# Optimization experiments

Hardware: AMD Instinct MI355X
Metric: run time of the kernel (lower is better)

## Reference

```python
import jax, jax.numpy as jnp
import numpy as np

B = 16384   # batch (agents x parallel envs)
IN = 12     # input_dim
H = 64      # hidden_dim -> 2H = 128
OUT = 25    # output_dim (forced by x[:,0:5]..x[:,20:25] slicing)


def setup_inputs() -> dict:
    key = jax.random.key(0)
    ks = jax.random.split(key, 24)
    n = lambda k, s: jax.random.normal(k, s, dtype=jnp.float32)
    s = 0.1  # scale params to keep SiLU/softmax in a sane range
    return {
        "x": n(ks[0], (B, IN)),
        "na": 4,
        # mlp_in: Linear(IN, 2H) + SiLU
        "W_in": n(ks[1], (2 * H, IN)) * s, "b_in": n(ks[2], (2 * H,)) * s,
        # first attention (2H)
        "Aq4": n(ks[3], (2 * H, 2 * H)) * s, "Bq4": n(ks[4], (2 * H,)) * s,
        "Ak4": n(ks[5], (2 * H, 2 * H)) * s, "Bk4": n(ks[6], (2 * H,)) * s,
        "Av4": n(ks[7], (2 * H, 2 * H)) * s, "Bv4": n(ks[8], (2 * H,)) * s,
        # mlp_hidden_4: Linear(2H, H) + SiLU
        "W_h": n(ks[9], (H, 2 * H)) * s, "b_h": n(ks[10], (H,)) * s,
        # second attention (H)
        "Aq7": n(ks[11], (H, H)) * s, "Bq7": n(ks[12], (H,)) * s,
        "Ak7": n(ks[13], (H, H)) * s, "Bk7": n(ks[14], (H,)) * s,
        "Av7": n(ks[15], (H, H)) * s, "Bv7": n(ks[16], (H,)) * s,
        # mlp_out: Linear(H, OUT) + SiLU
        "W_out": n(ks[17], (OUT, H)) * s, "b_out": n(ks[18], (OUT,)) * s,
    }


def _attn(h, Aq, Bq, Ak, Bk, Av, Bv):
    # h: [B, D]; torch does bmm(A, x^T)+B with x of shape [B,1,D] -> seq-len-1
    # attention, i.e. scores are an outer product q k^T of shape [B, D, D].
    q = jax.nn.silu(h @ Aq.T + Bq)                      # [B, D]
    k = jax.nn.silu(h @ Ak.T + Bk)                      # [B, D]
    v = jax.nn.silu(h @ Av.T + Bv)                      # [B, D]
    a = jax.nn.softmax(q[:, :, None] * k[:, None, :], axis=2)  # [B, D, D]
    return jax.nn.silu(jnp.einsum("bij,bj->bi", a, v))  # [B, D]


def reference(x, na, W_in, b_in, Aq4, Bq4, Ak4, Bk4, Av4, Bv4,
              W_h, b_h, Aq7, Bq7, Ak7, Bk7, Av7, Bv7, W_out, b_out):
    h = jax.nn.silu(x @ W_in.T + b_in)                  # [B, 2H]
    h = _attn(h, Aq4, Bq4, Ak4, Bk4, Av4, Bv4)          # [B, 2H]
    h = jax.nn.silu(h @ W_h.T + b_h)                    # [B, H]
    h = _attn(h, Aq7, Bq7, Ak7, Bk7, Av7, Bv7)          # [B, H]
    y = jax.nn.silu(h @ W_out.T + b_out)                # [B, 25]

    # block-diagonal quadratic-form assembly (l=2, kron with ones(1,2))
    M11 = jnp.sum(y[:, 0:5] ** 2, axis=1)               # [B]
    M12 = jnp.sum(y[:, 5:10] ** 2, axis=1)
    M21 = jnp.sum(y[:, 10:15] ** 2, axis=1)
    M22 = jnp.sum(y[:, 15:20] ** 2, axis=1)
    Mpp = jnp.sum(y[:, 20:25] ** 2, axis=1)             # [B]
    q = y[:, :4]                                        # [B, 4] = [q0,q1,q2,q3]
    # M = [[diag(M11), diag(M12)],[diag(M21), diag(M22)]] (each 2x2 diag)
    quad = (M11 * (q[:, 0] ** 2 + q[:, 1] ** 2)
            + (M12 + M21) * (q[:, 0] * q[:, 2] + q[:, 1] * q[:, 3])
            + M22 * (q[:, 2] ** 2 + q[:, 3] ** 2))
    return (quad + Mpp)[:, None]                        # [B, 1]
```

## Files before the change

kernel.cpp:

```cpp
#include <hip/hip_runtime.h>

#define RPW 4
#define WAVES 4
#define RPB (RPW * WAVES)
#define NM 14

using short8 = __attribute__((ext_vector_type(8))) short;
using f32x4  = __attribute__((ext_vector_type(4))) float;

#define LOG2E 1.4426950408889634f

static __device__ __forceinline__ float ex2(float x) { return __builtin_amdgcn_exp2f(x); }
static __device__ __forceinline__ float rcpf_(float x) { return __builtin_amdgcn_rcpf(x); }
static __device__ __forceinline__ float silu_(float x) {
    return x * rcpf_(1.0f + ex2(-x * LOG2E));
}
static __device__ __forceinline__ unsigned short bfhi(float x) {
    return (unsigned short)(__float_as_uint(x) >> 16);
}
static __device__ __forceinline__ unsigned short bfrn(float x) {
    unsigned u = __float_as_uint(x);
    return (unsigned short)((u + 0x7fffu + ((u >> 16) & 1u)) >> 16);
}
static __device__ __forceinline__ float bf2f(unsigned short h) {
    return __uint_as_float(((unsigned)h) << 16);
}

template <int CTRL>
static __device__ __forceinline__ float dpp_rot(float v) {
    return __uint_as_float(
        __builtin_amdgcn_update_dpp(0u, __float_as_uint(v), CTRL, 0xF, 0xF, true));
}
static __device__ __forceinline__ float rsum16(float v) {
    v += dpp_rot<0x128>(v);
    v += dpp_rot<0x124>(v);
    v += dpp_rot<0x122>(v);
    v += dpp_rot<0x121>(v);
    return v;
}

__constant__ float c_invfact[15] = {
    1.f, 1.f, 0.5f, 1.f/6, 1.f/24, 1.f/120, 1.f/720, 1.f/5040, 1.f/40320,
    1.f/362880, 1.f/3628800, 1.f/39916800, 1.f/479001600,
    1.f/6227020800.f, 1.f/87178291200.f};

template <int O, int I>
__device__ __forceinline__ void tr(const float* __restrict__ s, float* __restrict__ d,
                                   int t0, int stride) {
    for (int idx = t0; idx < O * I; idx += stride) {
        int o = idx / I, in = idx - o * I;
        d[in * O + o] = s[idx];
    }
}
template <int N>
__device__ __forceinline__ void cvt(const float* __restrict__ s,
                                    unsigned short* __restrict__ hi,
                                    unsigned short* __restrict__ lo,
                                    int t0, int stride) {
    for (int i = t0; i < N; i += stride) {
        float a = s[i];
        unsigned short h = bfhi(a);
        float r = a - bf2f(h);
        hi[i] = h;
        lo[i] = bfhi(r);
    }
}

__global__ void tweights(const float* __restrict__ s0, const float* __restrict__ s1,
                         const float* __restrict__ s2, const float* __restrict__ s3,
                         const float* __restrict__ s4, const float* __restrict__ s5,
                         const float* __restrict__ s6, const float* __restrict__ s7,
                         const float* __restrict__ s8, float* __restrict__ ws) {
    const int stride = gridDim.x * blockDim.x;
    const int t0 = blockIdx.x * blockDim.x + threadIdx.x;
    tr<128, 12>(s0, ws + 0, t0, stride);
    unsigned short* u4 = (unsigned short*)(ws + 1536);
    cvt<128 * 128>(s1, u4 + 0,     u4 + 16384, t0, stride);
    cvt<128 * 128>(s2, u4 + 32768, u4 + 49152, t0, stride);
    cvt<128 * 128>(s3, u4 + 65536, u4 + 81920, t0, stride);
    unsigned short* wh = (unsigned short*)(ws + 50688);
    cvt<64 * 128>(s4, wh + 0, wh + 8192, t0, stride);
    unsigned short* u7 = (unsigned short*)(ws + 58880);
    cvt<64 * 64>(s5, u7 + 0,     u7 + 4096,  t0, stride);
    cvt<64 * 64>(s6, u7 + 8192,  u7 + 12288, t0, stride);
    cvt<64 * 64>(s7, u7 + 16384, u7 + 20480, t0, stride);
    tr<25, 64>(s8, ws + 71168, t0, stride);
}

__global__ __launch_bounds__(256, 4) void fused_net(
    const float* __restrict__ x, const float* __restrict__ ws,
    const float* __restrict__ b_in,
    const float* __restrict__ Bq4, const float* __restrict__ Bk4, const float* __restrict__ Bv4,
    const float* __restrict__ b_h,
    const float* __restrict__ Bq7, const float* __restrict__ Bk7, const float* __restrict__ Bv7,
    const float* __restrict__ b_out,
    float* __restrict__ out) {
    __shared__ __align__(16) unsigned short hAhi[16][136], hAlo[16][136];
    __shared__ __align__(16) unsigned short h2hi[16][80],  h2lo[16][80];
    __shared__ __align__(16) float sQ[16][132];
    __shared__ __align__(16) unsigned short sKVb[16][132][2];
    __shared__ __align__(16) float h3T[WAVES][64][RPW];
    __shared__ __align__(16) float sXT[WAVES][12][RPW];
    __shared__ __align__(16) float sY[WAVES][RPW][26];

    const int tid = threadIdx.x;
    const int w = tid >> 6;
    const int l = tid & 63;
    const int row0 = blockIdx.x * RPB + w * RPW;
    const int m16 = l & 15, quad = l >> 4;
    const int g = l & 15, r = l >> 4;
    const int R = w * RPW + r;

    const float* WinT  = ws + 0;
    const float* WoutT = ws + 71168;

    if (l < 12 * RPW) {
        float v = x[row0 * 12 + l];
        int rr = l / 12, in = l - rr * 12;
        sXT[w][in][rr] = v;
    }

    {
        float2 bb = *(const float2*)&b_in[2 * l];
        float a0[RPW], a1[RPW];
        #pragma unroll
        for (int rr = 0; rr < RPW; rr++) { a0[rr] = bb.x; a1[rr] = bb.y; }
        #pragma unroll
        for (int in = 0; in < 12; in++) {
            float2 wv = *(const float2*)&WinT[in * 128 + 2 * l];
            float4 xr = *(const float4*)&sXT[w][in][0];
            a0[0] = fmaf(xr.x, wv.x, a0[0]); a1[0] = fmaf(xr.x, wv.y, a1[0]);
            a0[1] = fmaf(xr.y, wv.x, a0[1]); a1[1] = fmaf(xr.y, wv.y, a1[1]);
            a0[2] = fmaf(xr.z, wv.x, a0[2]); a1[2] = fmaf(xr.z, wv.y, a1[2]);
            a0[3] = fmaf(xr.w, wv.x, a0[3]); a1[3] = fmaf(xr.w, wv.y, a1[3]);
        }
        #pragma unroll
        for (int rr = 0; rr < RPW; rr++) {
            float h0 = silu_(a0[rr]), h1 = silu_(a1[rr]);
            unsigned short h0h = bfhi(h0), h1h = bfhi(h1);
            float r0 = h0 - bf2f(h0h), r1 = h1 - bf2f(h1h);
            *(unsigned*)&hAhi[w * 4 + rr][2 * l] = (unsigned)h0h | ((unsigned)h1h << 16);
            *(unsigned*)&hAlo[w * 4 + rr][2 * l] = (unsigned)bfhi(r0) | ((unsigned)bfhi(r1) << 16);
        }
    }
    __syncthreads();

    {
        short8 Ah[4], Al[4];
        #pragma unroll
        for (int kt = 0; kt < 4; kt++) {
            Ah[kt] = *(const short8*)&hAhi[m16][kt * 32 + quad * 8];
            Al[kt] = *(const short8*)&hAlo[m16][kt * 32 + quad * 8];
        }
        const unsigned short* u4 = (const unsigned short*)(ws + 1536);
        #pragma unroll
        for (int t = 0; t < 6; t++) {
            const int nt = w * 6 + t;
            const int mat = nt >> 3;
            const int n = (nt & 7) * 16 + m16;
            const float* bp = (mat == 0) ? Bq4 : (mat == 1) ? Bk4 : Bv4;
            float b = bp[n];
            f32x4 acc = {b, b, b, b};
            const unsigned short* Bh = u4 + mat * 32768 + n * 128;
            const unsigned short* Bl = Bh + 16384;
            #pragma unroll
            for (int kt = 0; kt < 4; kt++) {
                short8 bh = *(const short8*)&Bh[kt * 32 + quad * 8];
                short8 bl = *(const short8*)&Bl[kt * 32 + quad * 8];
                acc = __builtin_amdgcn_mfma_f32_16x16x32_bf16(Ah[kt], bh, acc, 0, 0, 0);
                acc = __builtin_amdgcn_mfma_f32_16x16x32_bf16(Ah[kt], bl, acc, 0, 0, 0);
                acc = __builtin_amdgcn_mfma_f32_16x16x32_bf16(Al[kt], bh, acc, 0, 0, 0);
            }
            #pragma unroll
            for (int reg = 0; reg < 4; reg++) {
                int row = quad * 4 + reg;
                float val = silu_(acc[reg]);
                if (mat == 0)      sQ[row][n] = val;
                else if (mat == 1) sKVb[row][n][0] = bfrn(val);
                else               sKVb[row][n][1] = bfrn(val);
            }
        }
    }
    __syncthreads();

    {
        float dmom[NM];
        float nmom[NM + 1];
        #pragma unroll
        for (int m = 0; m < NM; m++) dmom[m] = 0.f;
        #pragma unroll
        for (int m = 0; m <= NM; m++) nmom[m] = 0.f;
        uint4 u0 = *(const uint4*)&sKVb[R][g * 8][0];
        uint4 u1 = *(const uint4*)&sKVb[R][g * 8 + 4][0];
        unsigned us[8] = {u0.x, u0.y, u0.z, u0.w, u1.x, u1.y, u1.z, u1.w};
        #pragma unroll
        for (int jj = 0; jj < 8; jj++) {
            unsigned u = us[jj];
            float kf = __uint_as_float(u << 16);
            float vf = __uint_as_float(u & 0xffff0000u);
            nmom[0] += vf;
            float p = kf;
            dmom[0] += p; nmom[1] = fmaf(vf, p, nmom[1]);
            #pragma unroll
            for (int m = 1; m < NM; m++) {
                p *= kf;
                dmom[m] += p;
                nmom[m + 1] = fmaf(vf, p, nmom[m + 1]);
            }
        }
        #pragma unroll
        for (int m = 0; m < NM; m++) dmom[m] = rsum16(dmom[m]);
        #pragma unroll
        for (int m = 0; m <= NM; m++) nmom[m] = rsum16(nmom[m]);
        float cd[NM + 1], cn[NM + 1];
        cd[0] = 128.f; cn[0] = nmom[0];
        #pragma unroll
        for (int m = 1; m <= NM; m++) {
            cd[m] = dmom[m - 1] * c_invfact[m];
            cn[m] = nmom[m] * c_invfact[m];
        }
        float4 qa = *(const float4*)&sQ[R][g * 8];
        float4 qb = *(const float4*)&sQ[R][g * 8 + 4];
        float qs[8] = {qa.x, qa.y, qa.z, qa.w, qb.x, qb.y, qb.z, qb.w};
        unsigned hiw[4], low[4];
        #pragma unroll
        for (int i = 0; i < 8; i++) {
            float t = qs[i];
            float d = cd[NM], nn = cn[NM];
            #pragma unroll
            for (int m = NM - 1; m >= 0; m--) {
                d = fmaf(d, t, cd[m]);
                nn = fmaf(nn, t, cn[m]);
            }
            float o = silu_(nn * rcpf_(d));
            unsigned short oh = bfhi(o);
            unsigned short olo = bfhi(o - bf2f(oh));
            if (i & 1) { hiw[i >> 1] |= ((unsigned)oh) << 16; low[i >> 1] |= ((unsigned)olo) << 16; }
            else       { hiw[i >> 1] = oh; low[i >> 1] = olo; }
        }
        *(uint4*)&hAhi[R][g * 8] = make_uint4(hiw[0], hiw[1], hiw[2], hiw[3]);
        *(uint4*)&hAlo[R][g * 8] = make_uint4(low[0], low[1], low[2], low[3]);
    }
    __syncthreads();

    {
        short8 Ah[4], Al[4];
        #pragma unroll
        for (int kt = 0; kt < 4; kt++) {
            Ah[kt] = *(const short8*)&hAhi[m16][kt * 32 + quad * 8];
            Al[kt] = *(const short8*)&hAlo[m16][kt * 32 + quad * 8];
        }
        const unsigned short* whh = (const unsigned short*)(ws + 50688);
        const unsigned short* whl = whh + 8192;
        const int n = w * 16 + m16;
        float b = b_h[n];
        f32x4 acc = {b, b, b, b};
        #pragma unroll
        for (int kt = 0; kt < 4; kt++) {
            short8 bh = *(const short8*)&whh[n * 128 + kt * 32 + quad * 8];
            short8 bl = *(const short8*)&whl[n * 128 + kt * 32 + quad * 8];
            acc = __builtin_amdgcn_mfma_f32_16x16x32_bf16(Ah[kt], bh, acc, 0, 0, 0);
            acc = __builtin_amdgcn_mfma_f32_16x16x32_bf16(Ah[kt], bl, acc, 0, 0, 0);
            acc = __builtin_amdgcn_mfma_f32_16x16x32_bf16(Al[kt], bh, acc, 0, 0, 0);
        }
        #pragma unroll
        for (int reg = 0; reg < 4; reg++) {
            int row = quad * 4 + reg;
            float hv = silu_(acc[reg]);
            unsigned short hh = bfhi(hv);
            h2hi[row][n] = hh;
            h2lo[row][n] = bfhi(hv - bf2f(hh));
        }
    }
    __syncthreads();

    {
        short8 Ah[2], Al[2];
        #pragma unroll
        for (int kt = 0; kt < 2; kt++) {
            Ah[kt] = *(const short8*)&h2hi[m16][kt * 32 + quad * 8];
            Al[kt] = *(const short8*)&h2lo[m16][kt * 32 + quad * 8];
        }
        const unsigned short* u7 = (const unsigned short*)(ws + 58880);
        #pragma unroll
        for (int t = 0; t < 3; t++) {
            const int nt = w * 3 + t;
            const int mat = nt >> 2;
            const int n = (nt & 3) * 16 + m16;
            const float* bp = (mat == 0) ? Bq7 : (mat == 1) ? Bk7 : Bv7;
            float b = bp[n];
            f32x4 acc = {b, b, b, b};
            const unsigned short* Bh = u7 + mat * 8192 + n * 64;
            const unsigned short* Bl = Bh + 4096;
            #pragma unroll
            for (int kt = 0; kt < 2; kt++) {
                short8 bh = *(const short8*)&Bh[kt * 32 + quad * 8];
                short8 bl = *(const short8*)&Bl[kt * 32 + quad * 8];
                acc = __builtin_amdgcn_mfma_f32_16x16x32_bf16(Ah[kt], bh, acc, 0, 0, 0);
                acc = __builtin_amdgcn_mfma_f32_16x16x32_bf16(Ah[kt], bl, acc, 0, 0, 0);
                acc = __builtin_amdgcn_mfma_f32_16x16x32_bf16(Al[kt], bh, acc, 0, 0, 0);
            }
            #pragma unroll
            for (int reg = 0; reg < 4; reg++) {
                int row = quad * 4 + reg;
                float val = silu_(acc[reg]);
                if (mat == 0)      sQ[row][n] = val;
                else if (mat == 1) sKVb[row][n][0] = bfrn(val);
                else               sKVb[row][n][1] = bfrn(val);
            }
        }
    }
    __syncthreads();

    {
        float dmom[NM];
        float nmom[NM + 1];
        #pragma unroll
        for (int m = 0; m < NM; m++) dmom[m] = 0.f;
        #pragma unroll
        for (int m = 0; m <= NM; m++) nmom[m] = 0.f;
        uint4 u0 = *(const uint4*)&sKVb[R][g * 4][0];
        unsigned us[4] = {u0.x, u0.y, u0.z, u0.w};
        #pragma unroll
        for (int jj = 0; jj < 4; jj++) {
            unsigned u = us[jj];
            float kf = __uint_as_float(u << 16);
            float vf = __uint_as_float(u & 0xffff0000u);
            nmom[0] += vf;
            float p = kf;
            dmom[0] += p; nmom[1] = fmaf(vf, p, nmom[1]);
            #pragma unroll
            for (int m = 1; m < NM; m++) {
                p *= kf;
                dmom[m] += p;
                nmom[m + 1] = fmaf(vf, p, nmom[m + 1]);
            }
        }
        #pragma unroll
        for (int m = 0; m < NM; m++) dmom[m] = rsum16(dmom[m]);
        #pragma unroll
        for (int m = 0; m <= NM; m++) nmom[m] = rsum16(nmom[m]);
        float cd[NM + 1], cn[NM + 1];
        cd[0] = 64.f; cn[0] = nmom[0];
        #pragma unroll
        for (int m = 1; m <= NM; m++) {
            cd[m] = dmom[m - 1] * c_invfact[m];
            cn[m] = nmom[m] * c_invfact[m];
        }
        float4 qa = *(const float4*)&sQ[R][g * 4];
        float qs[4] = {qa.x, qa.y, qa.z, qa.w};
        #pragma unroll
        for (int i = 0; i < 4; i++) {
            float t = qs[i];
            float d = cd[NM], nn = cn[NM];
            #pragma unroll
            for (int m = NM - 1; m >= 0; m--) {
                d = fmaf(d, t, cd[m]);
                nn = fmaf(nn, t, cn[m]);
            }
            h3T[w][g * 4 + i][r] = silu_(nn * rcpf_(d));
        }
    }

    {
        const int o = l & 31;
        const int half = l >> 5;
        const int oc = (o < 25) ? o : 0;
        float y[RPW];
        float bb = (half == 0) ? b_out[oc] : 0.f;
        #pragma unroll
        for (int rr = 0; rr < RPW; rr++) y[rr] = bb;
        const int in0 = half * 32;
        #pragma unroll 4
        for (int i = 0; i < 32; i++) {
            int in = in0 + i;
            float wv = WoutT[in * 25 + oc];
            float4 xr = *(const float4*)&h3T[w][in][0];
            y[0] = fmaf(xr.x, wv, y[0]);
            y[1] = fmaf(xr.y, wv, y[1]);
            y[2] = fmaf(xr.z, wv, y[2]);
            y[3] = fmaf(xr.w, wv, y[3]);
        }
        #pragma unroll
        for (int rr = 0; rr < RPW; rr++) {
            float full = y[rr] + __shfl_xor(y[rr], 32, 64);
            if (l < 25) sY[w][rr][l] = silu_(full);
        }
    }

    if (l < RPW) {
        const int rr = l;
        float y[25];
        #pragma unroll
        for (int c = 0; c < 25; c++) y[c] = sY[w][rr][c];
        float M11 = 0.f, M12 = 0.f, M21 = 0.f, M22 = 0.f, Mpp = 0.f;
        #pragma unroll
        for (int c = 0; c < 5; c++) {
            M11 = fmaf(y[c], y[c], M11);
            M12 = fmaf(y[5 + c], y[5 + c], M12);
            M21 = fmaf(y[10 + c], y[10 + c], M21);
            M22 = fmaf(y[15 + c], y[15 + c], M22);
            Mpp = fmaf(y[20 + c], y[20 + c], Mpp);
        }
        float quad = M11 * (y[0] * y[0] + y[1] * y[1])
                   + (M12 + M21) * (y[0] * y[2] + y[1] * y[3])
                   + M22 * (y[2] * y[2] + y[3] * y[3]);
        out[row0 + rr] = quad + Mpp;
    }
}

extern "C" void kernel_launch(void* const* d_in, const int* in_sizes, int n_in,
                              void* d_out, int out_size, void* d_ws, size_t ws_size,
                              hipStream_t stream) {
    const float* x    = (const float*)d_in[0];
    const float* W_in = (const float*)d_in[2];
    const float* b_in = (const float*)d_in[3];
    const float* Aq4  = (const float*)d_in[4];
    const float* Bq4  = (const float*)d_in[5];
    const float* Ak4  = (const float*)d_in[6];
    const float* Bk4  = (const float*)d_in[7];
    const float* Av4  = (const float*)d_in[8];
    const float* Bv4  = (const float*)d_in[9];
    const float* W_h  = (const float*)d_in[10];
    const float* b_h  = (const float*)d_in[11];
    const float* Aq7  = (const float*)d_in[12];
    const float* Bq7  = (const float*)d_in[13];
    const float* Ak7  = (const float*)d_in[14];
    const float* Bk7  = (const float*)d_in[15];
    const float* Av7  = (const float*)d_in[16];
    const float* Bv7  = (const float*)d_in[17];
    const float* Wout = (const float*)d_in[18];
    const float* bout = (const float*)d_in[19];
    float* ws = (float*)d_ws;

    tweights<<<256, 256, 0, stream>>>(W_in, Aq4, Ak4, Av4, W_h, Aq7, Ak7, Av7, Wout, ws);

    const int B = in_sizes[0] / 12;
    const int grid = B / RPB;
    fused_net<<<grid, 256, 0, stream>>>(x, ws, b_in, Bq4, Bk4, Bv4,
                                        b_h, Bq7, Bk7, Bv7, bout, (float*)d_out);
}
```

Baseline: 134.7 us.

## Shrink blocks to two waves with eight rows and prefetch MFMA weight fragments

Blocks drop from 4 waves/16 rows to 2 waves/8 rows, doubling the grid. MFMA tiles now carry only 8 valid rows (duplicated via m16&7), and only half the lanes write results. The first weight fragments of each GEMM stage are prefetched early, and the W_h GEMM is merged into the preceding attention section behind an extra barrier. Accumulation is split across two accumulators to shorten MFMA dependency chains. This halves useful MFMA work per instruction, so total MFMA issue roughly doubles, traded for more blocks and better latency hiding.

```diff
diff --git a/kernel.cpp b/kernel.cpp
--- a/kernel.cpp
+++ b/kernel.cpp
@@ -1,7 +1,7 @@
 #include <hip/hip_runtime.h>
 
 #define RPW 4
-#define WAVES 4
+#define WAVES 2
 #define RPB (RPW * WAVES)
 #define NM 14
 
@@ -87,7 +87,7 @@
     tr<25, 64>(s8, ws + 71168, t0, stride);
 }
 
-__global__ __launch_bounds__(256, 4) void fused_net(
+__global__ __launch_bounds__(128, 4) void fused_net(
     const float* __restrict__ x, const float* __restrict__ ws,
     const float* __restrict__ b_in,
     const float* __restrict__ Bq4, const float* __restrict__ Bk4, const float* __restrict__ Bv4,
@@ -95,10 +95,10 @@
     const float* __restrict__ Bq7, const float* __restrict__ Bk7, const float* __restrict__ Bv7,
     const float* __restrict__ b_out,
     float* __restrict__ out) {
-    __shared__ __align__(16) unsigned short hAhi[16][136], hAlo[16][136];
-    __shared__ __align__(16) unsigned short h2hi[16][80],  h2lo[16][80];
-    __shared__ __align__(16) float sQ[16][132];
-    __shared__ __align__(16) unsigned short sKVb[16][132][2];
+    __shared__ __align__(16) unsigned short hAhi[8][136], hAlo[8][136];
+    __shared__ __align__(16) unsigned short h2hi[8][80],  h2lo[8][80];
+    __shared__ __align__(16) float sQ[8][132];
+    __shared__ __align__(16) unsigned short sKVb[8][132][2];
     __shared__ __align__(16) float h3T[WAVES][64][RPW];
     __shared__ __align__(16) float sXT[WAVES][12][RPW];
     __shared__ __align__(16) float sY[WAVES][RPW][26];
@@ -113,11 +113,26 @@
 
     const float* WinT  = ws + 0;
     const float* WoutT = ws + 71168;
+    const unsigned short* u4 = (const unsigned short*)(ws + 1536);
 
     if (l < 12 * RPW) {
         float v = x[row0 * 12 + l];
         int rr = l / 12, in = l - rr * 12;
         sXT[w][in][rr] = v;
+    }
+
+    short8 p2bh[4], p2bl[4];
+    {
+        const int nt = w * 12;
+        const int mat = nt >> 3;
+        const int n = (nt & 7) * 16 + m16;
+        const unsigned short* Bh = u4 + mat * 32768 + n * 128;
+        const unsigned short* Bl = Bh + 16384;
+        #pragma unroll
+        for (int kt = 0; kt < 4; kt++) {
+            p2bh[kt] = *(const short8*)&Bh[kt * 32 + quad * 8];
+            p2bl[kt] = *(const short8*)&Bl[kt * 32 + quad * 8];
+        }
     }
 
     {
@@ -149,41 +164,69 @@
         short8 Ah[4], Al[4];
         #pragma unroll
         for (int kt = 0; kt < 4; kt++) {
-            Ah[kt] = *(const short8*)&hAhi[m16][kt * 32 + quad * 8];
-            Al[kt] = *(const short8*)&hAlo[m16][kt * 32 + quad * 8];
-        }
-        const unsigned short* u4 = (const unsigned short*)(ws + 1536);
-        #pragma unroll
-        for (int t = 0; t < 6; t++) {
-            const int nt = w * 6 + t;
+            Ah[kt] = *(const short8*)&hAhi[m16 & 7][kt * 32 + quad * 8];
+            Al[kt] = *(const short8*)&hAlo[m16 & 7][kt * 32 + quad * 8];
+        }
+        #pragma unroll 4
+        for (int t = 0; t < 12; t++) {
+            const int nt = w * 12 + t;
             const int mat = nt >> 3;
             const int n = (nt & 7) * 16 + m16;
             const float* bp = (mat == 0) ? Bq4 : (mat == 1) ? Bk4 : Bv4;
             float b = bp[n];
-            f32x4 acc = {b, b, b, b};
+            f32x4 acc0 = {b, b, b, b};
+            f32x4 acc1 = {0.f, 0.f, 0.f, 0.f};
             const unsigned short* Bh = u4 + mat * 32768 + n * 128;
             const unsigned short* Bl = Bh + 16384;
+            short8 bh[4], bl[4];
+            if (t == 0) {
+                #pragma unroll
+                for (int kt = 0; kt < 4; kt++) { bh[kt] = p2bh[kt]; bl[kt] = p2bl[kt]; }
+            } else {
+                #pragma unroll
+                for (int kt = 0; kt < 4; kt++) {
+                    bh[kt] = *(const short8*)&Bh[kt * 32 + quad * 8];
+                    bl[kt] = *(const short8*)&Bl[kt * 32 + quad * 8];
+                }
+            }
             #pragma unroll
             for (int kt = 0; kt < 4; kt++) {
-                short8 bh = *(const short8*)&Bh[kt * 32 + quad * 8];
-                short8 bl = *(const short8*)&Bl[kt * 32 + quad * 8];
-                acc = __builtin_amdgcn_mfma_f32_16x16x32_bf16(Ah[kt], bh, acc, 0, 0, 0);
-                acc = __builtin_amdgcn_mfma_f32_16x16x32_bf16(Ah[kt], bl, acc, 0, 0, 0);
-                acc = __builtin_amdgcn_mfma_f32_16x16x32_bf16(Al[kt], bh, acc, 0, 0, 0);
-            }
-            #pragma unroll
-            for (int reg = 0; reg < 4; reg++) {
-                int row = quad * 4 + reg;
-                float val = silu_(acc[reg]);
-                if (mat == 0)      sQ[row][n] = val;
-                else if (mat == 1) sKVb[row][n][0] = bfrn(val);
-                else               sKVb[row][n][1] = bfrn(val);
+                if (kt & 1) {
+                    acc1 = __builtin_amdgcn_mfma_f32_16x16x32_bf16(Ah[kt], bh[kt], acc1, 0, 0, 0);
+                    acc1 = __builtin_amdgcn_mfma_f32_16x16x32_bf16(Ah[kt], bl[kt], acc1, 0, 0, 0);
+                    acc1 = __builtin_amdgcn_mfma_f32_16x16x32_bf16(Al[kt], bh[kt], acc1, 0, 0, 0);
+                } else {
+                    acc0 = __builtin_amdgcn_mfma_f32_16x16x32_bf16(Ah[kt], bh[kt], acc0, 0, 0, 0);
+                    acc0 = __builtin_amdgcn_mfma_f32_16x16x32_bf16(Ah[kt], bl[kt], acc0, 0, 0, 0);
+                    acc0 = __builtin_amdgcn_mfma_f32_16x16x32_bf16(Al[kt], bh[kt], acc0, 0, 0, 0);
+                }
+            }
+            if (quad < 2) {
+                #pragma unroll
+                for (int reg = 0; reg < 4; reg++) {
+                    int row = quad * 4 + reg;
+                    float val = silu_(acc0[reg] + acc1[reg]);
+                    if (mat == 0)      sQ[row][n] = val;
+                    else if (mat == 1) sKVb[row][n][0] = bfrn(val);
+                    else               sKVb[row][n][1] = bfrn(val);
+                }
             }
         }
     }
     __syncthreads();
 
     {
+        short8 p4bh[4], p4bl[4];
+        const unsigned short* whh = (const unsigned short*)(ws + 50688);
+        const unsigned short* whl = whh + 8192;
+        {
+            const int n4 = (w * 2) * 16 + m16;
+            #pragma unroll
+            for (int kt = 0; kt < 4; kt++) {
+                p4bh[kt] = *(const short8*)&whh[n4 * 128 + kt * 32 + quad * 8];
+                p4bl[kt] = *(const short8*)&whl[n4 * 128 + kt * 32 + quad * 8];
+            }
+        }
         float dmom[NM];
         float nmom[NM + 1];
         #pragma unroll
@@ -240,73 +283,95 @@
         }
         *(uint4*)&hAhi[R][g * 8] = make_uint4(hiw[0], hiw[1], hiw[2], hiw[3]);
         *(uint4*)&hAlo[R][g * 8] = make_uint4(low[0], low[1], low[2], low[3]);
+        __syncthreads();
+
+        short8 Ah[4], Al[4];
+        #pragma unroll
+        for (int kt = 0; kt < 4; kt++) {
+            Ah[kt] = *(const short8*)&hAhi[m16 & 7][kt * 32 + quad * 8];
+            Al[kt] = *(const short8*)&hAlo[m16 & 7][kt * 32 + quad * 8];
+        }
+        #pragma unroll
+        for (int t = 0; t < 2; t++) {
+            const int n = (w * 2 + t) * 16 + m16;
+            short8 bh[4], bl[4];
+            if (t == 0) {
+                #pragma unroll
+                for (int kt = 0; kt < 4; kt++) { bh[kt] = p4bh[kt]; bl[kt] = p4bl[kt]; }
+            } else {
+                #pragma unroll
+                for (int kt = 0; kt < 4; kt++) {
+                    bh[kt] = *(const short8*)&whh[n * 128 + kt * 32 + quad * 8];
+                    bl[kt] = *(const short8*)&whl[n * 128 + kt * 32 + quad * 8];
+                }
+            }
+            float b = b_h[n];
+            f32x4 acc0 = {b, b, b, b};
+            f32x4 acc1 = {0.f, 0.f, 0.f, 0.f};
+            #pragma unroll
+            for (int kt = 0; kt < 4; kt++) {
+                if (kt & 1) {
+                    acc1 = __builtin_amdgcn_mfma_f32_16x16x32_bf16(Ah[kt], bh[kt], acc1, 0, 0, 0);
+                    acc1 = __builtin_amdgcn_mfma_f32_16x16x32_bf16(Ah[kt], bl[kt], acc1, 0, 0, 0);
+                    acc1 = __builtin_amdgcn_mfma_f32_16x16x32_bf16(Al[kt], bh[kt], acc1, 0, 0, 0);
+                } else {
+                    acc0 = __builtin_amdgcn_mfma_f32_16x16x32_bf16(Ah[kt], bh[kt], acc0, 0, 0, 0);
+                    acc0 = __builtin_amdgcn_mfma_f32_16x16x32_bf16(Ah[kt], bl[kt], acc0, 0, 0, 0);
+                    acc0 = __builtin_amdgcn_mfma_f32_16x16x32_bf16(Al[kt], bh[kt], acc0, 0, 0, 0);
+                }
+            }
+            if (quad < 2) {
+                #pragma unroll
+                for (int reg = 0; reg < 4; reg++) {
+                    int row = quad * 4 + reg;
+                    float hv = silu_(acc0[reg] + acc1[reg]);
+                    unsigned short hh = bfhi(hv);
+                    h2hi[row][n] = hh;
+                    h2lo[row][n] = bfhi(hv - bf2f(hh));
+                }
+            }
+        }
     }
     __syncthreads();
 
     {
-        short8 Ah[4], Al[4];
-        #pragma unroll
-        for (int kt = 0; kt < 4; kt++) {
-            Ah[kt] = *(const short8*)&hAhi[m16][kt * 32 + quad * 8];
-            Al[kt] = *(const short8*)&hAlo[m16][kt * 32 + quad * 8];
-        }
-        const unsigned short* whh = (const unsigned short*)(ws + 50688);
-        const unsigned short* whl = whh + 8192;
-        const int n = w * 16 + m16;
-        float b = b_h[n];
-        f32x4 acc = {b, b, b, b};
-        #pragma unroll
-        for (int kt = 0; kt < 4; kt++) {
-            short8 bh = *(const short8*)&whh[n * 128 + kt * 32 + quad * 8];
-            short8 bl = *(const short8*)&whl[n * 128 + kt * 32 + quad * 8];
-            acc = __builtin_amdgcn_mfma_f32_16x16x32_bf16(Ah[kt], bh, acc, 0, 0, 0);
-            acc = __builtin_amdgcn_mfma_f32_16x16x32_bf16(Ah[kt], bl, acc, 0, 0, 0);
-            acc = __builtin_amdgcn_mfma_f32_16x16x32_bf16(Al[kt], bh, acc, 0, 0, 0);
-        }
-        #pragma unroll
-        for (int reg = 0; reg < 4; reg++) {
-            int row = quad * 4 + reg;
-            float hv = silu_(acc[reg]);
-            unsigned short hh = bfhi(hv);
-            h2hi[row][n] = hh;
-            h2lo[row][n] = bfhi(hv - bf2f(hh));
-        }
-    }
-    __syncthreads();
-
-    {
+        const unsigned short* u7 = (const unsigned short*)(ws + 58880);
         short8 Ah[2], Al[2];
         #pragma unroll
         for (int kt = 0; kt < 2; kt++) {
-            Ah[kt] = *(const short8*)&h2hi[m16][kt * 32 + quad * 8];
-            Al[kt] = *(const short8*)&h2lo[m16][kt * 32 + quad * 8];
-        }
-        const unsigned short* u7 = (const unsigned short*)(ws + 58880);
-        #pragma unroll
-        for (int t = 0; t < 3; t++) {
-            const int nt = w * 3 + t;
+            Ah[kt] = *(const short8*)&h2hi[m16 & 7][kt * 32 + quad * 8];
+            Al[kt] = *(const short8*)&h2lo[m16 & 7][kt * 32 + quad * 8];
+        }
+        #pragma unroll 3
+        for (int t = 0; t < 6; t++) {
+            const int nt = w * 6 + t;
             const int mat = nt >> 2;
             const int n = (nt & 3) * 16 + m16;
             const float* bp = (mat == 0) ? Bq7 : (mat == 1) ? Bk7 : Bv7;
             float b = bp[n];
-            f32x4 acc = {b, b, b, b};
+            f32x4 acc0 = {b, b, b, b};
+            f32x4 acc1 = {0.f, 0.f, 0.f, 0.f};
             const unsigned short* Bh = u7 + mat * 8192 + n * 64;
             const unsigned short* Bl = Bh + 4096;
-            #pragma unroll
-            for (int kt = 0; kt < 2; kt++) {
-                short8 bh = *(const short8*)&Bh[kt * 32 + quad * 8];
-                short8 bl = *(const short8*)&Bl[kt * 32 + quad * 8];
-                acc = __builtin_amdgcn_mfma_f32_16x16x32_bf16(Ah[kt], bh, acc, 0, 0, 0);
-                acc = __builtin_amdgcn_mfma_f32_16x16x32_bf16(Ah[kt], bl, acc, 0, 0, 0);
-                acc = __builtin_amdgcn_mfma_f32_16x16x32_bf16(Al[kt], bh, acc, 0, 0, 0);
-            }
-            #pragma unroll
-            for (int reg = 0; reg < 4; reg++) {
-                int row = quad * 4 + reg;
-                float val = silu_(acc[reg]);
-                if (mat == 0)      sQ[row][n] = val;
-                else if (mat == 1) sKVb[row][n][0] = bfrn(val);
-                else               sKVb[row][n][1] = bfrn(val);
+            short8 bh0 = *(const short8*)&Bh[quad * 8];
+            short8 bl0 = *(const short8*)&Bl[quad * 8];
+            short8 bh1 = *(const short8*)&Bh[32 + quad * 8];
+            short8 bl1 = *(const short8*)&Bl[32 + quad * 8];
+            acc0 = __builtin_amdgcn_mfma_f32_16x16x32_bf16(Ah[0], bh0, acc0, 0, 0, 0);
+            acc1 = __builtin_amdgcn_mfma_f32_16x16x32_bf16(Ah[1], bh1, acc1, 0, 0, 0);
+            acc0 = __builtin_amdgcn_mfma_f32_16x16x32_bf16(Ah[0], bl0, acc0, 0, 0, 0);
+            acc1 = __builtin_amdgcn_mfma_f32_16x16x32_bf16(Ah[1], bl1, acc1, 0, 0, 0);
+            acc0 = __builtin_amdgcn_mfma_f32_16x16x32_bf16(Al[0], bh0, acc0, 0, 0, 0);
+            acc1 = __builtin_amdgcn_mfma_f32_16x16x32_bf16(Al[1], bh1, acc1, 0, 0, 0);
+            if (quad < 2) {
+                #pragma unroll
+                for (int reg = 0; reg < 4; reg++) {
+                    int row = quad * 4 + reg;
+                    float val = silu_(acc0[reg] + acc1[reg]);
+                    if (mat == 0)      sQ[row][n] = val;
+                    else if (mat == 1) sKVb[row][n][0] = bfrn(val);
+                    else               sKVb[row][n][1] = bfrn(val);
+                }
             }
         }
     }
@@ -402,10 +467,10 @@
             M22 = fmaf(y[15 + c], y[15 + c], M22);
             Mpp = fmaf(y[20 + c], y[20 + c], Mpp);
         }
-        float quad = M11 * (y[0] * y[0] + y[1] * y[1])
-                   + (M12 + M21) * (y[0] * y[2] + y[1] * y[3])
-                   + M22 * (y[2] * y[2] + y[3] * y[3]);
-        out[row0 + rr] = quad + Mpp;
+        float quad_ = M11 * (y[0] * y[0] + y[1] * y[1])
+                    + (M12 + M21) * (y[0] * y[2] + y[1] * y[3])
+                    + M22 * (y[2] * y[2] + y[3] * y[3]);
+        out[row0 + rr] = quad_ + Mpp;
     }
 }
 
@@ -437,6 +502,6 @@
 
     const int B = in_sizes[0] / 12;
     const int grid = B / RPB;
-    fused_net<<<grid, 256, 0, stream>>>(x, ws, b_in, Bq4, Bk4, Bv4,
+    fused_net<<<grid, 128, 0, stream>>>(x, ws, b_in, Bq4, Bk4, Bv4,
                                         b_h, Bq7, Bk7, Bv7, bout, (float*)d_out);
 }
```

New measurement: 163.2 us. 21.2% more time.

## Interleave two 16-row groups per block to overlap MFMA and moment phases

Applied to the files above, without the earlier changes.

Each block now processes two 16-row groups with double-buffered shared memory, and a skewed schedule runs the MFMA phase of one group alongside the scalar moment/polynomial phase of the other between barriers. MFMA chains are split into two accumulators to shorten dependency chains. The Taylor moment order is reduced from 14 to 12, and launch bounds are relaxed to 2 blocks per SM, giving more registers but halving the grid. The risks are lower occupancy, doubled LDS use, and reduced accuracy of the truncated series.

```diff
diff --git a/kernel.cpp b/kernel.cpp
--- a/kernel.cpp
+++ b/kernel.cpp
@@ -1,9 +1,6 @@
 #include <hip/hip_runtime.h>
 
-#define RPW 4
-#define WAVES 4
-#define RPB (RPW * WAVES)
-#define NM 14
+#define NM 12
 
 using short8 = __attribute__((ext_vector_type(8))) short;
 using f32x4  = __attribute__((ext_vector_type(4))) float;
@@ -39,10 +36,11 @@
     return v;
 }
 
-__constant__ float c_invfact[15] = {
+__constant__ float c_invfact[13] = {
     1.f, 1.f, 0.5f, 1.f/6, 1.f/24, 1.f/120, 1.f/720, 1.f/5040, 1.f/40320,
-    1.f/362880, 1.f/3628800, 1.f/39916800, 1.f/479001600,
-    1.f/6227020800.f, 1.f/87178291200.f};
+    1.f/362880, 1.f/3628800, 1.f/39916800, 1.f/479001600};
+
+#define MFMA16(A, B, C) __builtin_amdgcn_mfma_f32_16x16x32_bf16((A), (B), (C), 0, 0, 0)
 
 template <int O, int I>
 __device__ __forceinline__ void tr(const float* __restrict__ s, float* __restrict__ d,
@@ -87,7 +85,7 @@
     tr<25, 64>(s8, ws + 71168, t0, stride);
 }
 
-__global__ __launch_bounds__(256, 4) void fused_net(
+__global__ __launch_bounds__(256, 2) void fused_net(
     const float* __restrict__ x, const float* __restrict__ ws,
     const float* __restrict__ b_in,
     const float* __restrict__ Bq4, const float* __restrict__ Bk4, const float* __restrict__ Bv4,
@@ -95,64 +93,67 @@
     const float* __restrict__ Bq7, const float* __restrict__ Bk7, const float* __restrict__ Bv7,
     const float* __restrict__ b_out,
     float* __restrict__ out) {
-    __shared__ __align__(16) unsigned short hAhi[16][136], hAlo[16][136];
-    __shared__ __align__(16) unsigned short h2hi[16][80],  h2lo[16][80];
-    __shared__ __align__(16) float sQ[16][132];
-    __shared__ __align__(16) unsigned short sKVb[16][132][2];
-    __shared__ __align__(16) float h3T[WAVES][64][RPW];
-    __shared__ __align__(16) float sXT[WAVES][12][RPW];
-    __shared__ __align__(16) float sY[WAVES][RPW][26];
+    __shared__ __align__(16) unsigned short hAhi[2][16][136], hAlo[2][16][136];
+    __shared__ __align__(16) unsigned short h2hi[2][16][80],  h2lo[2][16][80];
+    __shared__ __align__(16) float sQ[2][16][132];
+    __shared__ __align__(16) unsigned short sKVb[2][16][132][2];
+    __shared__ __align__(16) float h3T[2][4][64][4];
+    __shared__ __align__(16) float sXT[2][4][12][4];
+    __shared__ __align__(16) float sY[2][4][4][26];
 
     const int tid = threadIdx.x;
     const int w = tid >> 6;
     const int l = tid & 63;
-    const int row0 = blockIdx.x * RPB + w * RPW;
+    const int row0 = blockIdx.x * 32;
     const int m16 = l & 15, quad = l >> 4;
     const int g = l & 15, r = l >> 4;
-    const int R = w * RPW + r;
+    const int R = w * 4 + r;
 
     const float* WinT  = ws + 0;
     const float* WoutT = ws + 71168;
-
-    if (l < 12 * RPW) {
-        float v = x[row0 * 12 + l];
-        int rr = l / 12, in = l - rr * 12;
-        sXT[w][in][rr] = v;
-    }
-
-    {
+    const unsigned short* u4  = (const unsigned short*)(ws + 1536);
+    const unsigned short* whh = (const unsigned short*)(ws + 50688);
+    const unsigned short* whl = whh + 8192;
+    const unsigned short* u7  = (const unsigned short*)(ws + 58880);
+
+    auto stageX = [&](int G) {
+        if (l < 48) {
+            int rr = l / 12, in = l - rr * 12;
+            sXT[G][w][in][rr] = x[(row0 + G * 16 + w * 4 + rr) * 12 + in];
+        }
+    };
+
+    auto phase1 = [&](int G) {
         float2 bb = *(const float2*)&b_in[2 * l];
-        float a0[RPW], a1[RPW];
-        #pragma unroll
-        for (int rr = 0; rr < RPW; rr++) { a0[rr] = bb.x; a1[rr] = bb.y; }
+        float a0[4], a1[4];
+        #pragma unroll
+        for (int rr = 0; rr < 4; rr++) { a0[rr] = bb.x; a1[rr] = bb.y; }
         #pragma unroll
         for (int in = 0; in < 12; in++) {
             float2 wv = *(const float2*)&WinT[in * 128 + 2 * l];
-            float4 xr = *(const float4*)&sXT[w][in][0];
+            float4 xr = *(const float4*)&sXT[G][w][in][0];
             a0[0] = fmaf(xr.x, wv.x, a0[0]); a1[0] = fmaf(xr.x, wv.y, a1[0]);
             a0[1] = fmaf(xr.y, wv.x, a0[1]); a1[1] = fmaf(xr.y, wv.y, a1[1]);
             a0[2] = fmaf(xr.z, wv.x, a0[2]); a1[2] = fmaf(xr.z, wv.y, a1[2]);
             a0[3] = fmaf(xr.w, wv.x, a0[3]); a1[3] = fmaf(xr.w, wv.y, a1[3]);
         }
         #pragma unroll
-        for (int rr = 0; rr < RPW; rr++) {
+        for (int rr = 0; rr < 4; rr++) {
             float h0 = silu_(a0[rr]), h1 = silu_(a1[rr]);
             unsigned short h0h = bfhi(h0), h1h = bfhi(h1);
             float r0 = h0 - bf2f(h0h), r1 = h1 - bf2f(h1h);
-            *(unsigned*)&hAhi[w * 4 + rr][2 * l] = (unsigned)h0h | ((unsigned)h1h << 16);
-            *(unsigned*)&hAlo[w * 4 + rr][2 * l] = (unsigned)bfhi(r0) | ((unsigned)bfhi(r1) << 16);
-        }
-    }
-    __syncthreads();
-
-    {
+            *(unsigned*)&hAhi[G][w * 4 + rr][2 * l] = (unsigned)h0h | ((unsigned)h1h << 16);
+            *(unsigned*)&hAlo[G][w * 4 + rr][2 * l] = (unsigned)bfhi(r0) | ((unsigned)bfhi(r1) << 16);
+        }
+    };
+
+    auto phase2 = [&](int G) {
         short8 Ah[4], Al[4];
         #pragma unroll
         for (int kt = 0; kt < 4; kt++) {
-            Ah[kt] = *(const short8*)&hAhi[m16][kt * 32 + quad * 8];
-            Al[kt] = *(const short8*)&hAlo[m16][kt * 32 + quad * 8];
-        }
-        const unsigned short* u4 = (const unsigned short*)(ws + 1536);
+            Ah[kt] = *(const short8*)&hAhi[G][m16][kt * 32 + quad * 8];
+            Al[kt] = *(const short8*)&hAlo[G][m16][kt * 32 + quad * 8];
+        }
         #pragma unroll
         for (int t = 0; t < 6; t++) {
             const int nt = w * 6 + t;
@@ -160,38 +161,43 @@
             const int n = (nt & 7) * 16 + m16;
             const float* bp = (mat == 0) ? Bq4 : (mat == 1) ? Bk4 : Bv4;
             float b = bp[n];
-            f32x4 acc = {b, b, b, b};
+            f32x4 acc0 = {b, b, b, b};
+            f32x4 acc1 = {0.f, 0.f, 0.f, 0.f};
             const unsigned short* Bh = u4 + mat * 32768 + n * 128;
             const unsigned short* Bl = Bh + 16384;
             #pragma unroll
             for (int kt = 0; kt < 4; kt++) {
                 short8 bh = *(const short8*)&Bh[kt * 32 + quad * 8];
                 short8 bl = *(const short8*)&Bl[kt * 32 + quad * 8];
-                acc = __builtin_amdgcn_mfma_f32_16x16x32_bf16(Ah[kt], bh, acc, 0, 0, 0);
-                acc = __builtin_amdgcn_mfma_f32_16x16x32_bf16(Ah[kt], bl, acc, 0, 0, 0);
-                acc = __builtin_amdgcn_mfma_f32_16x16x32_bf16(Al[kt], bh, acc, 0, 0, 0);
+                if (kt & 1) {
+                    acc1 = MFMA16(Ah[kt], bh, acc1);
+                    acc1 = MFMA16(Ah[kt], bl, acc1);
+                    acc1 = MFMA16(Al[kt], bh, acc1);
+                } else {
+                    acc0 = MFMA16(Ah[kt], bh, acc0);
+                    acc0 = MFMA16(Ah[kt], bl, acc0);
+                    acc0 = MFMA16(Al[kt], bh, acc0);
+                }
             }
             #pragma unroll
             for (int reg = 0; reg < 4; reg++) {
                 int row = quad * 4 + reg;
-                float val = silu_(acc[reg]);
-                if (mat == 0)      sQ[row][n] = val;
-                else if (mat == 1) sKVb[row][n][0] = bfrn(val);
-                else               sKVb[row][n][1] = bfrn(val);
-            }
-        }
-    }
-    __syncthreads();
-
-    {
-        float dmom[NM];
-        float nmom[NM + 1];
+                float val = silu_(acc0[reg] + acc1[reg]);
+                if (mat == 0)      sQ[G][row][n] = val;
+                else if (mat == 1) sKVb[G][row][n][0] = bfrn(val);
+                else               sKVb[G][row][n][1] = bfrn(val);
+            }
+        }
+    };
+
+    auto phase3 = [&](int G) {
+        float dmom[NM], nmom[NM + 1];
         #pragma unroll
         for (int m = 0; m < NM; m++) dmom[m] = 0.f;
         #pragma unroll
         for (int m = 0; m <= NM; m++) nmom[m] = 0.f;
-        uint4 u0 = *(const uint4*)&sKVb[R][g * 8][0];
-        uint4 u1 = *(const uint4*)&sKVb[R][g * 8 + 4][0];
+        uint4 u0 = *(const uint4*)&sKVb[G][R][g * 8][0];
+        uint4 u1 = *(const uint4*)&sKVb[G][R][g * 8 + 4][0];
         unsigned us[8] = {u0.x, u0.y, u0.z, u0.w, u1.x, u1.y, u1.z, u1.w};
         #pragma unroll
         for (int jj = 0; jj < 8; jj++) {
@@ -219,8 +225,8 @@
             cd[m] = dmom[m - 1] * c_invfact[m];
             cn[m] = nmom[m] * c_invfact[m];
         }
-        float4 qa = *(const float4*)&sQ[R][g * 8];
-        float4 qb = *(const float4*)&sQ[R][g * 8 + 4];
+        float4 qa = *(const float4*)&sQ[G][R][g * 8];
+        float4 qb = *(const float4*)&sQ[G][R][g * 8 + 4];
         float qs[8] = {qa.x, qa.y, qa.z, qa.w, qb.x, qb.y, qb.z, qb.w};
         unsigned hiw[4], low[4];
         #pragma unroll
@@ -238,50 +244,52 @@
             if (i & 1) { hiw[i >> 1] |= ((unsigned)oh) << 16; low[i >> 1] |= ((unsigned)olo) << 16; }
             else       { hiw[i >> 1] = oh; low[i >> 1] = olo; }
         }
-        *(uint4*)&hAhi[R][g * 8] = make_uint4(hiw[0], hiw[1], hiw[2], hiw[3]);
-        *(uint4*)&hAlo[R][g * 8] = make_uint4(low[0], low[1], low[2], low[3]);
-    }
-    __syncthreads();
-
-    {
+        *(uint4*)&hAhi[G][R][g * 8] = make_uint4(hiw[0], hiw[1], hiw[2], hiw[3]);
+        *(uint4*)&hAlo[G][R][g * 8] = make_uint4(low[0], low[1], low[2], low[3]);
+    };
+
+    auto phase4 = [&](int G) {
         short8 Ah[4], Al[4];
         #pragma unroll
         for (int kt = 0; kt < 4; kt++) {
-            Ah[kt] = *(const short8*)&hAhi[m16][kt * 32 + quad * 8];
-            Al[kt] = *(const short8*)&hAlo[m16][kt * 32 + quad * 8];
-        }
-        const unsigned short* whh = (const unsigned short*)(ws + 50688);
-        const unsigned short* whl = whh + 8192;
+            Ah[kt] = *(const short8*)&hAhi[G][m16][kt * 32 + quad * 8];
+            Al[kt] = *(const short8*)&hAlo[G][m16][kt * 32 + quad * 8];
+        }
         const int n = w * 16 + m16;
         float b = b_h[n];
-        f32x4 acc = {b, b, b, b};
+        f32x4 acc0 = {b, b, b, b};
+        f32x4 acc1 = {0.f, 0.f, 0.f, 0.f};
         #pragma unroll
         for (int kt = 0; kt < 4; kt++) {
             short8 bh = *(const short8*)&whh[n * 128 + kt * 32 + quad * 8];
             short8 bl = *(const short8*)&whl[n * 128 + kt * 32 + quad * 8];
-            acc = __builtin_amdgcn_mfma_f32_16x16x32_bf16(Ah[kt], bh, acc, 0, 0, 0);
-            acc = __builtin_amdgcn_mfma_f32_16x16x32_bf16(Ah[kt], bl, acc, 0, 0, 0);
-            acc = __builtin_amdgcn_mfma_f32_16x16x32_bf16(Al[kt], bh, acc, 0, 0, 0);
+            if (kt & 1) {
+                acc1 = MFMA16(Ah[kt], bh, acc1);
+                acc1 = MFMA16(Ah[kt], bl, acc1);
+                acc1 = MFMA16(Al[kt], bh, acc1);
+            } else {
+                acc0 = MFMA16(Ah[kt], bh, acc0);
+                acc0 = MFMA16(Ah[kt], bl, acc0);
+                acc0 = MFMA16(Al[kt], bh, acc0);
+            }
         }
         #pragma unroll
         for (int reg = 0; reg < 4; reg++) {
             int row = quad * 4 + reg;
-            float hv = silu_(acc[reg]);
+            float hv = silu_(acc0[reg] + acc1[reg]);
             unsigned short hh = bfhi(hv);
-            h2hi[row][n] = hh;
-            h2lo[row][n] = bfhi(hv - bf2f(hh));
-        }
-    }
-    __syncthreads();
-
-    {
+            h2hi[G][row][n] = hh;
+            h2lo[G][row][n] = bfhi(hv - bf2f(hh));
+        }
+    };
+
+    auto phase5 = [&](int G) {
         short8 Ah[2], Al[2];
         #pragma unroll
         for (int kt = 0; kt < 2; kt++) {
-            Ah[kt] = *(const short8*)&h2hi[m16][kt * 32 + quad * 8];
-            Al[kt] = *(const short8*)&h2lo[m16][kt * 32 + quad * 8];
-        }
-        const unsigned short* u7 = (const unsigned short*)(ws + 58880);
+            Ah[kt] = *(const short8*)&h2hi[G][m16][kt * 32 + quad * 8];
+            Al[kt] = *(const short8*)&h2lo[G][m16][kt * 32 + quad * 8];
+        }
         #pragma unroll
         for (int t = 0; t < 3; t++) {
             const int nt = w * 3 + t;
@@ -289,37 +297,38 @@
             const int n = (nt & 3) * 16 + m16;
             const float* bp = (mat == 0) ? Bq7 : (mat == 1) ? Bk7 : Bv7;
             float b = bp[n];
-            f32x4 acc = {b, b, b, b};
+            f32x4 acc0 = {b, b, b, b};
+            f32x4 acc1 = {0.f, 0.f, 0.f, 0.f};
             const unsigned short* Bh = u7 + mat * 8192 + n * 64;
             const unsigned short* Bl = Bh + 4096;
-            #pragma unroll
-            for (int kt = 0; kt < 2; kt++) {
-                short8 bh = *(const short8*)&Bh[kt * 32 + quad * 8];
-                short8 bl = *(const short8*)&Bl[kt * 32 + quad * 8];
-                acc = __builtin_amdgcn_mfma_f32_16x16x32_bf16(Ah[kt], bh, acc, 0, 0, 0);
-                acc = __builtin_amdgcn_mfma_f32_16x16x32_bf16(Ah[kt], bl, acc, 0, 0, 0);
-                acc = __builtin_amdgcn_mfma_f32_16x16x32_bf16(Al[kt], bh, acc, 0, 0, 0);
-            }
+            short8 bh0 = *(const short8*)&Bh[quad * 8];
+            short8 bl0 = *(const short8*)&Bl[quad * 8];
+            short8 bh1 = *(const short8*)&Bh[32 + quad * 8];
+            short8 bl1 = *(const short8*)&Bl[32 + quad * 8];
+            acc0 = MFMA16(Ah[0], bh0, acc0);
+            acc1 = MFMA16(Ah[1], bh1, acc1);
+            acc0 = MFMA16(Ah[0], bl0, acc0);
+            acc1 = MFMA16(Ah[1], bl1, acc1);
+            acc0 = MFMA16(Al[0], bh0, acc0);
+            acc1 = MFMA16(Al[1], bh1, acc1);
             #pragma unroll
             for (int reg = 0; reg < 4; reg++) {
                 int row = quad * 4 + reg;
-                float val = silu_(acc[reg]);
-                if (mat == 0)      sQ[row][n] = val;
-                else if (mat == 1) sKVb[row][n][0] = bfrn(val);
-                else               sKVb[row][n][1] = bfrn(val);
-            }
-        }
-    }
-    __syncthreads();
-
-    {
-        float dmom[NM];
-        float nmom[NM + 1];
+                float val = silu_(acc0[reg] + acc1[reg]);
+                if (mat == 0)      sQ[G][row][n] = val;
+                else if (mat == 1) sKVb[G][row][n][0] = bfrn(val);
+                else               sKVb[G][row][n][1] = bfrn(val);
+            }
+        }
+    };
+
+    auto phase6 = [&](int G) {
+        float dmom[NM], nmom[NM + 1];
         #pragma unroll
         for (int m = 0; m < NM; m++) dmom[m] = 0.f;
         #pragma unroll
         for (int m = 0; m <= NM; m++) nmom[m] = 0.f;
-        uint4 u0 = *(const uint4*)&sKVb[R][g * 4][0];
+        uint4 u0 = *(const uint4*)&sKVb[G][R][g * 4][0];
         unsigned us[4] = {u0.x, u0.y, u0.z, u0.w};
         #pragma unroll
         for (int jj = 0; jj < 4; jj++) {
@@ -347,7 +356,7 @@
             cd[m] = dmom[m - 1] * c_invfact[m];
             cn[m] = nmom[m] * c_invfact[m];
         }
-        float4 qa = *(const float4*)&sQ[R][g * 4];
+        float4 qa = *(const float4*)&sQ[G][R][g * 4];
         float qs[4] = {qa.x, qa.y, qa.z, qa.w};
         #pragma unroll
         for (int i = 0; i < 4; i++) {
@@ -358,55 +367,72 @@
                 d = fmaf(d, t, cd[m]);
                 nn = fmaf(nn, t, cn[m]);
             }
-            h3T[w][g * 4 + i][r] = silu_(nn * rcpf_(d));
-        }
-    }
-
-    {
-        const int o = l & 31;
-        const int half = l >> 5;
-        const int oc = (o < 25) ? o : 0;
-        float y[RPW];
-        float bb = (half == 0) ? b_out[oc] : 0.f;
-        #pragma unroll
-        for (int rr = 0; rr < RPW; rr++) y[rr] = bb;
-        const int in0 = half * 32;
-        #pragma unroll 4
-        for (int i = 0; i < 32; i++) {
-            int in = in0 + i;
-            float wv = WoutT[in * 25 + oc];
-            float4 xr = *(const float4*)&h3T[w][in][0];
-            y[0] = fmaf(xr.x, wv, y[0]);
-            y[1] = fmaf(xr.y, wv, y[1]);
-            y[2] = fmaf(xr.z, wv, y[2]);
-            y[3] = fmaf(xr.w, wv, y[3]);
-        }
-        #pragma unroll
-        for (int rr = 0; rr < RPW; rr++) {
-            float full = y[rr] + __shfl_xor(y[rr], 32, 64);
-            if (l < 25) sY[w][rr][l] = silu_(full);
-        }
-    }
-
-    if (l < RPW) {
-        const int rr = l;
-        float y[25];
-        #pragma unroll
-        for (int c = 0; c < 25; c++) y[c] = sY[w][rr][c];
-        float M11 = 0.f, M12 = 0.f, M21 = 0.f, M22 = 0.f, Mpp = 0.f;
-        #pragma unroll
-        for (int c = 0; c < 5; c++) {
-            M11 = fmaf(y[c], y[c], M11);
-            M12 = fmaf(y[5 + c], y[5 + c], M12);
-            M21 = fmaf(y[10 + c], y[10 + c], M21);
-            M22 = fmaf(y[15 + c], y[15 + c], M22);
-            Mpp = fmaf(y[20 + c], y[20 + c], Mpp);
-        }
-        float quad = M11 * (y[0] * y[0] + y[1] * y[1])
-                   + (M12 + M21) * (y[0] * y[2] + y[1] * y[3])
-                   + M22 * (y[2] * y[2] + y[3] * y[3]);
-        out[row0 + rr] = quad + Mpp;
-    }
+            h3T[G][w][g * 4 + i][r] = silu_(nn * rcpf_(d));
+        }
+    };
+
+    auto phase78 = [&](int G) {
+        {
+            const int o = l & 31;
+            const int half = l >> 5;
+            const int oc = (o < 25) ? o : 0;
+            float y[4];
+            float bb = (half == 0) ? b_out[oc] : 0.f;
+            #pragma unroll
+            for (int rr = 0; rr < 4; rr++) y[rr] = bb;
+            const int in0 = half * 32;
+            #pragma unroll 4
+            for (int i = 0; i < 32; i++) {
+                int in = in0 + i;
+                float wv = WoutT[in * 25 + oc];
+                float4 xr = *(const float4*)&h3T[G][w][in][0];
+                y[0] = fmaf(xr.x, wv, y[0]);
+                y[1] = fmaf(xr.y, wv, y[1]);
+                y[2] = fmaf(xr.z, wv, y[2]);
+                y[3] = fmaf(xr.w, wv, y[3]);
+            }
+            #pragma unroll
+            for (int rr = 0; rr < 4; rr++) {
+                float full = y[rr] + __shfl_xor(y[rr], 32, 64);
+                if (l < 25) sY[G][w][rr][l] = silu_(full);
+            }
+        }
+        if (l < 4) {
+            const int rr = l;
+            float y[25];
+            #pragma unroll
+            for (int c = 0; c < 25; c++) y[c] = sY[G][w][rr][c];
+            float M11 = 0.f, M12 = 0.f, M21 = 0.f, M22 = 0.f, Mpp = 0.f;
+            #pragma unroll
+            for (int c = 0; c < 5; c++) {
+                M11 = fmaf(y[c], y[c], M11);
+                M12 = fmaf(y[5 + c], y[5 + c], M12);
+                M21 = fmaf(y[10 + c], y[10 + c], M21);
+                M22 = fmaf(y[15 + c], y[15 + c], M22);
+                Mpp = fmaf(y[20 + c], y[20 + c], Mpp);
+            }
+            float quad_ = M11 * (y[0] * y[0] + y[1] * y[1])
+                        + (M12 + M21) * (y[0] * y[2] + y[1] * y[3])
+                        + M22 * (y[2] * y[2] + y[3] * y[3]);
+            out[row0 + G * 16 + w * 4 + rr] = quad_ + Mpp;
+        }
+    };
+
+    stageX(0); stageX(1);
+    phase1(0);
+    __syncthreads();
+    phase2(0); phase1(1);
+    __syncthreads();
+    phase2(1); phase3(0);
+    __syncthreads();
+    phase4(0); phase3(1);
+    __syncthreads();
+    phase5(0); phase4(1);
+    __syncthreads();
+    phase5(1); phase6(0);
+    __syncthreads();
+    phase78(0); phase6(1);
+    phase78(1);
 }
 
 extern "C" void kernel_launch(void* const* d_in, const int* in_sizes, int n_in,
@@ -436,7 +462,7 @@
     tweights<<<256, 256, 0, stream>>>(W_in, Aq4, Ak4, Av4, W_h, Aq7, Ak7, Av7, Wout, ws);
 
     const int B = in_sizes[0] / 12;
-    const int grid = B / RPB;
+    const int grid = B / 32;
     fused_net<<<grid, 256, 0, stream>>>(x, ws, b_in, Bq4, Bk4, Bv4,
                                         b_h, Bq7, Bk7, Bv7, bout, (float*)d_out);
 }
```

Result: slower. 151.3 us (+12.3%).
